# Kernel tuning notes

Measured on AMD Instinct MI355X. Metric: run time of the kernel, lower is better.

## Reference

```python
import jax, jax.numpy as jnp
import numpy as np

B, S, D, H, MLP_D = 2, 2048, 512, 8, 128
DH = D // H  # 64
EPS = 1e-5


def setup_inputs() -> dict:
    key = jax.random.key(0)
    ks = jax.random.split(key, 8)
    return {
        "z": jax.random.normal(ks[0], (B, S, D), dtype=jnp.float32),
        "head_w": jax.random.normal(ks[1], (H, D, 3 * DH), dtype=jnp.float32),
        "w_o": jax.random.normal(ks[2], (H * DH, D), dtype=jnp.float32),
        "ln_w": jnp.ones((D,), dtype=jnp.float32),
        "ln_b": jnp.zeros((D,), dtype=jnp.float32),
        "w1": jax.random.normal(ks[3], (D, MLP_D), dtype=jnp.float32) * (1.0 / np.sqrt(D)),
        "b1": jnp.zeros((MLP_D,), dtype=jnp.float32),
        "w2": jax.random.normal(ks[4], (MLP_D, D), dtype=jnp.float32) * (1.0 / np.sqrt(MLP_D)),
        "b2": jnp.zeros((D,), dtype=jnp.float32),
    }


def _layernorm(x, w, b):
    mu = jnp.mean(x, axis=-1, keepdims=True)
    var = jnp.var(x, axis=-1, keepdims=True)
    return (x - mu) * jax.lax.rsqrt(var + EPS) * w + b


def reference(z, head_w, w_o, ln_w, ln_b, w1, b1, w2, b2):
    # --- MSA block: z = MSA(LN(z)) + z ---
    x = _layernorm(z, ln_w, ln_b)                       # [B,S,D]
    qkv = jnp.einsum("bsd,hde->bhse", x, head_w)        # [B,H,S,3*DH]
    q, k, v = qkv[..., :DH], qkv[..., DH:2 * DH], qkv[..., 2 * DH:]
    scores = jnp.einsum("bhsd,bhtd->bhst", q, k) / jnp.sqrt(jnp.float32(DH))
    p = jax.nn.softmax(scores, axis=-1)                 # [B,H,S,S]
    o = jnp.einsum("bhst,bhtd->bhsd", p, v)             # [B,H,S,DH]
    # concat heads along last dim (head order matches torch.cat), then project
    o = jnp.transpose(o, (0, 2, 1, 3)).reshape(B, S, H * DH)
    z = o @ w_o + z
    # --- MLP block: z = GELU(Linear2(Linear1(LN(z)))) + z (GELU last, per Sequential) ---
    y = _layernorm(z, ln_w, ln_b)
    y = (y @ w1 + b1) @ w2 + b2
    z = jax.nn.gelu(y, approximate=False) + z
    return z
```

## Files before the change

### kernel.cpp

```cpp
#include <hip/hip_runtime.h>
#include <hip/hip_bf16.h>

typedef unsigned short u16;
typedef unsigned int u32;
typedef __attribute__((ext_vector_type(8))) short short8;
typedef __attribute__((ext_vector_type(8))) __bf16 bf16x8;
typedef __attribute__((ext_vector_type(4))) float f32x4;

#define DEV static __device__ __forceinline__

DEV float bf2f(u16 u) { unsigned v = ((unsigned)u) << 16; float f; __builtin_memcpy(&f, &v, 4); return f; }
DEV u16 f2bf(float f) {
  unsigned u; __builtin_memcpy(&u, &f, 4);
  unsigned lsb = (u >> 16) & 1;
  u += 0x7fffu + lsb;
  return (u16)(u >> 16);
}
DEV u16 tbf(float f) {
  unsigned u; __builtin_memcpy(&u, &f, 4);
  return (u16)(u >> 16);
}
DEV float exp2fast(float x) { return __builtin_amdgcn_exp2f(x); }
DEV f32x4 mfma16(short8 a, short8 b, f32x4 c) {
  return __builtin_amdgcn_mfma_f32_16x16x32_bf16(
      __builtin_bit_cast(bf16x8, a), __builtin_bit_cast(bf16x8, b), c, 0, 0, 0);
}
DEV short8 ld8(const u16* p) { return *(const short8*)p; }

__global__ void prep_all(const float* __restrict__ hw, const float* __restrict__ wo,
                         const float* __restrict__ w1, const float* __restrict__ w2,
                         u16* __restrict__ wqh, u16* __restrict__ wql,
                         u16* __restrict__ woT, u16* __restrict__ w1T, u16* __restrict__ w2T) {
  int idx = blockIdx.x * 256 + threadIdx.x;
  if (idx < 786432) {
    int e = idx % 192;
    int d = (idx / 192) % 512;
    int h = idx / (192 * 512);
    float v = hw[idx];
    int n = (e < 64) ? (h * 64 + e) : (e < 128) ? (512 + h * 64 + e - 64) : (1024 + h * 64 + e - 128);
    size_t oi = (size_t)n * 512 + d;
    u16 hh = f2bf(v);
    wqh[oi] = hh;
    if (e < 128) wql[oi] = f2bf(v - bf2f(hh));
  } else if (idx < 786432 + 262144) {
    int i = idx - 786432;
    int n = i % 512, k = i / 512;
    woT[(size_t)n * 512 + k] = f2bf(wo[i]);
  } else if (idx < 786432 + 262144 + 65536) {
    int i = idx - (786432 + 262144);
    int n = i % 128, k = i / 128;
    w1T[(size_t)n * 512 + k] = f2bf(w1[i]);
  } else if (idx < 786432 + 262144 + 131072) {
    int i = idx - (786432 + 262144 + 65536);
    int n = i % 512, k = i / 512;
    w2T[(size_t)n * 128 + k] = f2bf(w2[i]);
  }
}

__global__ __launch_bounds__(256) void ln_kernel(const float* __restrict__ in,
                                                 const float* __restrict__ w,
                                                 const float* __restrict__ bb,
                                                 u16* __restrict__ hi, u16* __restrict__ lo) {
  const int wv = threadIdx.x >> 6, lane = threadIdx.x & 63;
  const int row = blockIdx.x * 4 + wv;
  const float4* r = (const float4*)(in + (size_t)row * 512);
  float4 a0 = r[lane * 2], a1 = r[lane * 2 + 1];
  float s = a0.x + a0.y + a0.z + a0.w + a1.x + a1.y + a1.z + a1.w;
  float ss = a0.x * a0.x + a0.y * a0.y + a0.z * a0.z + a0.w * a0.w +
             a1.x * a1.x + a1.y * a1.y + a1.z * a1.z + a1.w * a1.w;
#pragma unroll
  for (int m = 1; m < 64; m <<= 1) { s += __shfl_xor(s, m); ss += __shfl_xor(ss, m); }
  float mu = s * (1.f / 512.f);
  float var = ss * (1.f / 512.f) - mu * mu;
  float rstd = rsqrtf(var + 1e-5f);
  const float4* wp = (const float4*)w + lane * 2;
  const float4* bp = (const float4*)bb + lane * 2;
  float4 w0 = wp[0], w1v = wp[1], b0 = bp[0], b1v = bp[1];
  float xv[8] = {a0.x, a0.y, a0.z, a0.w, a1.x, a1.y, a1.z, a1.w};
  float wv8[8] = {w0.x, w0.y, w0.z, w0.w, w1v.x, w1v.y, w1v.z, w1v.w};
  float bv8[8] = {b0.x, b0.y, b0.z, b0.w, b1v.x, b1v.y, b1v.z, b1v.w};
  short8 oh, ol;
#pragma unroll
  for (int i = 0; i < 8; i++) {
    float v = (xv[i] - mu) * rstd * wv8[i] + bv8[i];
    u16 hh = f2bf(v);
    oh[i] = (short)hh;
    ol[i] = (short)f2bf(v - bf2f(hh));
  }
  *(short8*)(hi + (size_t)row * 512 + lane * 8) = oh;
  *(short8*)(lo + (size_t)row * 512 + lane * 8) = ol;
}

__global__ __launch_bounds__(256) void gemm_qkv(const u16* __restrict__ Ah, const u16* __restrict__ Alo,
                                                const u16* __restrict__ Bh, const u16* __restrict__ Blo,
                                                u16* __restrict__ qkh, u16* __restrict__ qkl,
                                                u16* __restrict__ vT) {
  __shared__ __align__(16) u16 As[128][40], Asl[128][40], Bs[64][40], Bsl[64][40];
  const int tid = threadIdx.x, lane = tid & 63, wv = tid >> 6;
  const int wm = wv >> 1, wn = wv & 1, g = lane >> 4, r16 = lane & 15;
  const int bm = blockIdx.x * 128, bn = blockIdx.y * 64;
  const bool split = blockIdx.y < 16;
  short8 sA[2], sAl[2], sB, sBl;
  auto ldtile = [&](int kt) {
#pragma unroll
    for (int c = 0; c < 2; c++) {
      int ch = c * 256 + tid;
      sA[c] = ld8(Ah + (size_t)(bm + (ch >> 2)) * 512 + kt + (ch & 3) * 8);
      if (split) sAl[c] = ld8(Alo + (size_t)(bm + (ch >> 2)) * 512 + kt + (ch & 3) * 8);
    }
    sB = ld8(Bh + (size_t)(bn + (tid >> 2)) * 512 + kt + (tid & 3) * 8);
    if (split) sBl = ld8(Blo + (size_t)(bn + (tid >> 2)) * 512 + kt + (tid & 3) * 8);
  };
  f32x4 acc[4][2] = {};
  ldtile(0);
  for (int kt = 0; kt < 512; kt += 32) {
    __syncthreads();
#pragma unroll
    for (int c = 0; c < 2; c++) {
      int ch = c * 256 + tid;
      *(short8*)&As[ch >> 2][(ch & 3) * 8] = sA[c];
      if (split) *(short8*)&Asl[ch >> 2][(ch & 3) * 8] = sAl[c];
    }
    *(short8*)&Bs[tid >> 2][(tid & 3) * 8] = sB;
    if (split) *(short8*)&Bsl[tid >> 2][(tid & 3) * 8] = sBl;
    __syncthreads();
    if (kt + 32 < 512) ldtile(kt + 32);
    short8 af[4], bf_[2], afl[4], bfl[2];
#pragma unroll
    for (int mi = 0; mi < 4; mi++) af[mi] = *(const short8*)&As[wm * 64 + mi * 16 + r16][g * 8];
#pragma unroll
    for (int ni = 0; ni < 2; ni++) bf_[ni] = *(const short8*)&Bs[wn * 32 + ni * 16 + r16][g * 8];
    if (split) {
#pragma unroll
      for (int mi = 0; mi < 4; mi++) afl[mi] = *(const short8*)&Asl[wm * 64 + mi * 16 + r16][g * 8];
#pragma unroll
      for (int ni = 0; ni < 2; ni++) bfl[ni] = *(const short8*)&Bsl[wn * 32 + ni * 16 + r16][g * 8];
    }
#pragma unroll
    for (int mi = 0; mi < 4; mi++)
#pragma unroll
      for (int ni = 0; ni < 2; ni++) {
        acc[mi][ni] = mfma16(af[mi], bf_[ni], acc[mi][ni]);
        if (split) {
          acc[mi][ni] = mfma16(af[mi], bfl[ni], acc[mi][ni]);
          acc[mi][ni] = mfma16(afl[mi], bf_[ni], acc[mi][ni]);
        }
      }
  }
#pragma unroll
  for (int mi = 0; mi < 4; mi++)
#pragma unroll
    for (int ni = 0; ni < 2; ni++) {
      int col = bn + wn * 32 + ni * 16 + r16;
      int row0 = bm + wm * 64 + mi * 16 + g * 4;
      if (split) {
#pragma unroll
        for (int j = 0; j < 4; j++) {
          size_t oi = (size_t)(row0 + j) * 1024 + col;
          float v = acc[mi][ni][j];
          u16 hh = f2bf(v);
          qkh[oi] = hh;
          qkl[oi] = f2bf(v - bf2f(hh));
        }
      } else {
        int vcol = col - 1024;
        ushort4 pk;
        pk.x = f2bf(acc[mi][ni][0]);
        pk.y = f2bf(acc[mi][ni][1]);
        pk.z = f2bf(acc[mi][ni][2]);
        pk.w = f2bf(acc[mi][ni][3]);
        *(ushort4*)(vT + (size_t)vcol * 4096 + row0) = pk;
      }
    }
}

template <int MF, int NF, int EPI>
__global__ __launch_bounds__(256) void gemm_g(const u16* __restrict__ A, const u16* __restrict__ BT,
                                              const float* __restrict__ res, const float* __restrict__ bias,
                                              u16* __restrict__ outb, float* __restrict__ outf,
                                              int N, int K) {
  constexpr int BM = 32 * MF, BN = 32 * NF;
  constexpr int CA = (BM * 4 + 255) / 256, CB = (BN * 4 + 255) / 256;
  __shared__ __align__(16) u16 As[BM][40], Bs[BN][40];
  const int tid = threadIdx.x, lane = tid & 63, wv = tid >> 6;
  const int wm = wv >> 1, wn = wv & 1, g = lane >> 4, r16 = lane & 15;
  const int bm = blockIdx.x * BM, bn = blockIdx.y * BN;
  short8 sA[CA], sB[CB];
  auto ldtile = [&](int kt) {
#pragma unroll
    for (int c = 0; c < CA; c++) {
      int ch = c * 256 + tid;
      if (ch < BM * 4) sA[c] = ld8(A + (size_t)(bm + (ch >> 2)) * K + kt + (ch & 3) * 8);
    }
#pragma unroll
    for (int c = 0; c < CB; c++) {
      int ch = c * 256 + tid;
      if (ch < BN * 4) sB[c] = ld8(BT + (size_t)(bn + (ch >> 2)) * K + kt + (ch & 3) * 8);
    }
  };
  f32x4 acc[MF][NF] = {};
  ldtile(0);
  for (int kt = 0; kt < K; kt += 32) {
    __syncthreads();
#pragma unroll
    for (int c = 0; c < CA; c++) {
      int ch = c * 256 + tid;
      if (ch < BM * 4) *(short8*)&As[ch >> 2][(ch & 3) * 8] = sA[c];
    }
#pragma unroll
    for (int c = 0; c < CB; c++) {
      int ch = c * 256 + tid;
      if (ch < BN * 4) *(short8*)&Bs[ch >> 2][(ch & 3) * 8] = sB[c];
    }
    __syncthreads();
    if (kt + 32 < K) ldtile(kt + 32);
    short8 af[MF], bf_[NF];
#pragma unroll
    for (int mi = 0; mi < MF; mi++) af[mi] = *(const short8*)&As[wm * 16 * MF + mi * 16 + r16][g * 8];
#pragma unroll
    for (int ni = 0; ni < NF; ni++) bf_[ni] = *(const short8*)&Bs[wn * 16 * NF + ni * 16 + r16][g * 8];
#pragma unroll
    for (int mi = 0; mi < MF; mi++)
#pragma unroll
      for (int ni = 0; ni < NF; ni++) acc[mi][ni] = mfma16(af[mi], bf_[ni], acc[mi][ni]);
  }
#pragma unroll
  for (int mi = 0; mi < MF; mi++)
#pragma unroll
    for (int ni = 0; ni < NF; ni++) {
      int col = bn + wn * 16 * NF + ni * 16 + r16;
      int row0 = bm + wm * 16 * MF + mi * 16 + g * 4;
#pragma unroll
      for (int j = 0; j < 4; j++) {
        size_t oi = (size_t)(row0 + j) * N + col;
        float v = acc[mi][ni][j];
        if (EPI == 1) {
          outf[oi] = v + res[oi];
        } else if (EPI == 2) {
          outb[oi] = f2bf(v + bias[col]);
        } else {
          float u = v + bias[col];
          float gl = 0.5f * u * (1.0f + erff(u * 0.70710678118f));
          outf[oi] = gl + res[oi];
        }
      }
    }
}

__global__ __launch_bounds__(256) void attn_kernel(const u16* __restrict__ qkh,
                                                   const u16* __restrict__ qkl,
                                                   const u16* __restrict__ vT,
                                                   u16* __restrict__ o) {
  constexpr int SK = 72, SV = 136, SP = 136;
  __shared__ __align__(16) u16 Kh[128 * SK], Kl[128 * SK], Vt[64 * SV];
  __shared__ __align__(16) u16 Pl[4][16 * SP];
  const int tid = threadIdx.x, lane = tid & 63, w = tid >> 6;
  const int g = lane >> 4, r16 = lane & 15;
  const int qb = blockIdx.x * 64;
  const int b = blockIdx.y >> 3, h = blockIdx.y & 7;
  const size_t bbase = (size_t)b * 2048 * 1024;
  const u16* Qh = qkh + bbase + h * 64;
  const u16* Ql = qkl + bbase + h * 64;
  const u16* KgH = qkh + bbase + 512 + h * 64;
  const u16* KgL = qkl + bbase + 512 + h * 64;
  const u16* Vtg = vT + (size_t)h * 64 * 4096 + (size_t)b * 2048;

  const int qrow = qb + w * 16 + r16;
  short8 qh[2], qlo[2];
#pragma unroll
  for (int ks = 0; ks < 2; ks++) {
    qh[ks] = ld8(Qh + (size_t)qrow * 1024 + ks * 32 + g * 8);
    qlo[ks] = ld8(Ql + (size_t)qrow * 1024 + ks * 32 + g * 8);
  }

  f32x4 oacc[4] = {};
  float m_r = -3e38f, l_r = 0.f;

  const int vd0 = tid >> 4, vkv = (tid & 15) * 8;
  short8 kA[4], kB[4], vS[4];
  auto ldkv = [&](int kt) {
#pragma unroll
    for (int c = 0; c < 4; c++) {
      int ch = c * 256 + tid;
      int kr = ch >> 3, kc = (ch & 7) * 8;
      kA[c] = ld8(KgH + (size_t)(kt + kr) * 1024 + kc);
      kB[c] = ld8(KgL + (size_t)(kt + kr) * 1024 + kc);
    }
#pragma unroll
    for (int c = 0; c < 4; c++)
      vS[c] = ld8(Vtg + (size_t)(vd0 + c * 16) * 4096 + kt + vkv);
  };
  ldkv(0);

  for (int kt = 0; kt < 2048; kt += 128) {
    __syncthreads();
#pragma unroll
    for (int c = 0; c < 4; c++) {
      int ch = c * 256 + tid;
      int kr = ch >> 3, kc = (ch & 7) * 8;
      *(short8*)&Kh[kr * SK + kc] = kA[c];
      *(short8*)&Kl[kr * SK + kc] = kB[c];
    }
#pragma unroll
    for (int c = 0; c < 4; c++)
      *(short8*)&Vt[(vd0 + c * 16) * SV + vkv] = vS[c];
    __syncthreads();
    if (kt + 128 < 2048) ldkv(kt + 128);
    f32x4 s[8];
#pragma unroll
    for (int f = 0; f < 8; f++) {
      s[f] = f32x4{0.f, 0.f, 0.f, 0.f};
#pragma unroll
      for (int ks = 0; ks < 2; ks++) {
        short8 bh = *(const short8*)&Kh[(f * 16 + r16) * SK + ks * 32 + g * 8];
        short8 bl = *(const short8*)&Kl[(f * 16 + r16) * SK + ks * 32 + g * 8];
        s[f] = mfma16(bh, qh[ks], s[f]);
        s[f] = mfma16(bl, qh[ks], s[f]);
        s[f] = mfma16(bh, qlo[ks], s[f]);
      }
    }
    constexpr float SCL2 = 0.125f * 1.44269504f;
    float a[8][4];
    float vm = -3e38f;
#pragma unroll
    for (int f = 0; f < 8; f++)
#pragma unroll
      for (int r = 0; r < 4; r++) {
        a[f][r] = s[f][r] * SCL2;
        vm = fmaxf(vm, a[f][r]);
      }
    vm = fmaxf(vm, __shfl_xor(vm, 16));
    vm = fmaxf(vm, __shfl_xor(vm, 32));
    float mn = fmaxf(m_r, vm);
    float scl = exp2fast(m_r - mn);
    m_r = mn;
    float rs = 0.f;
#pragma unroll
    for (int f = 0; f < 8; f++) {
      float e0 = exp2fast(a[f][0] - mn), e1 = exp2fast(a[f][1] - mn);
      float e2 = exp2fast(a[f][2] - mn), e3 = exp2fast(a[f][3] - mn);
      rs += (e0 + e1) + (e2 + e3);
      u32 u0, u1, u2, u3;
      __builtin_memcpy(&u0, &e0, 4);
      __builtin_memcpy(&u1, &e1, 4);
      __builtin_memcpy(&u2, &e2, 4);
      __builtin_memcpy(&u3, &e3, 4);
      uint2 pk;
      pk.x = (u0 >> 16) | (u1 & 0xFFFF0000u);
      pk.y = (u2 >> 16) | (u3 & 0xFFFF0000u);
      *(uint2*)&Pl[w][r16 * SP + f * 16 + g * 4] = pk;
    }
    rs += __shfl_xor(rs, 16);
    rs += __shfl_xor(rs, 32);
    l_r = l_r * scl + rs;
#pragma unroll
    for (int j = 0; j < 4; j++) {
      float sj = __shfl(scl, (g << 4) + (g << 2) + j);
#pragma unroll
      for (int dt = 0; dt < 4; dt++) oacc[dt][j] *= sj;
    }
#pragma unroll
    for (int ks = 0; ks < 4; ks++) {
      short8 pa = *(const short8*)&Pl[w][r16 * SP + ks * 32 + g * 8];
#pragma unroll
      for (int dt = 0; dt < 4; dt++) {
        short8 vb = *(const short8*)&Vt[(dt * 16 + r16) * SV + ks * 32 + g * 8];
        oacc[dt] = mfma16(pa, vb, oacc[dt]);
      }
    }
  }
#pragma unroll
  for (int j = 0; j < 4; j++) {
    float lj = __shfl(l_r, (g << 4) + (g << 2) + j);
    float il = 1.f / lj;
    int row = b * 2048 + qb + w * 16 + g * 4 + j;
#pragma unroll
    for (int dt = 0; dt < 4; dt++) {
      int col = h * 64 + dt * 16 + r16;
      o[(size_t)row * 512 + col] = f2bf(oacc[dt][j] * il);
    }
  }
}

extern "C" void kernel_launch(void* const* d_in, const int* in_sizes, int n_in,
                              void* d_out, int out_size, void* d_ws, size_t ws_size,
                              hipStream_t stream) {
  const float* z = (const float*)d_in[0];
  const float* head_w = (const float*)d_in[1];
  const float* w_o = (const float*)d_in[2];
  const float* ln_w = (const float*)d_in[3];
  const float* ln_b = (const float*)d_in[4];
  const float* w1 = (const float*)d_in[5];
  const float* b1 = (const float*)d_in[6];
  const float* w2 = (const float*)d_in[7];
  const float* b2 = (const float*)d_in[8];
  float* out = (float*)d_out;

  size_t off = 0;
  auto alc = [&](size_t n) {
    void* p = (char*)d_ws + off;
    off += (n + 255) & ~(size_t)255;
    return p;
  };
  u16* x_hi = (u16*)alc((size_t)4096 * 512 * 2);
  u16* x_lo = (u16*)alc((size_t)4096 * 512 * 2);
  u16* wqh = (u16*)alc((size_t)1536 * 512 * 2);
  u16* wql = (u16*)alc((size_t)1536 * 512 * 2);
  u16* woT = (u16*)alc((size_t)512 * 512 * 2);
  u16* w1T = (u16*)alc((size_t)128 * 512 * 2);
  u16* w2T = (u16*)alc((size_t)512 * 128 * 2);
  u16* qkh = (u16*)alc((size_t)4096 * 1024 * 2);
  u16* qkl = (u16*)alc((size_t)4096 * 1024 * 2);
  u16* vT = (u16*)alc((size_t)512 * 4096 * 2);
  u16* ob = (u16*)alc((size_t)4096 * 512 * 2);
  float* z2 = (float*)alc((size_t)4096 * 512 * 4);
  u16* tb = (u16*)alc((size_t)4096 * 128 * 2);

  prep_all<<<4608, 256, 0, stream>>>(head_w, w_o, w1, w2, wqh, wql, woT, w1T, w2T);

  ln_kernel<<<1024, 256, 0, stream>>>(z, ln_w, ln_b, x_hi, x_lo);

  gemm_qkv<<<dim3(32, 24), 256, 0, stream>>>(x_hi, x_lo, wqh, wql, qkh, qkl, vT);

  attn_kernel<<<dim3(32, 16), 256, 0, stream>>>(qkh, qkl, vT, ob);

  gemm_g<2, 2, 1><<<dim3(64, 8), 256, 0, stream>>>(ob, woT, z, nullptr, nullptr, z2, 512, 512);

  ln_kernel<<<1024, 256, 0, stream>>>(z2, ln_w, ln_b, x_hi, x_lo);

  gemm_g<1, 2, 2><<<dim3(128, 2), 256, 0, stream>>>(x_hi, w1T, nullptr, b1, tb, nullptr, 128, 512);

  gemm_g<2, 2, 3><<<dim3(64, 8), 256, 0, stream>>>(tb, w2T, z2, b2, nullptr, out, 512, 128);
}
```

Measured before the change: 128.2 us.

## Process two query tiles per wave in attention to reuse K/V fragments

Attention blocks shrink from 4 waves to 2, and each wave now handles 32 query rows as two 16-row tiles. Each K and V fragment read from LDS then feeds two sets of MFMAs, halving LDS reads per MFMA. The cost is about double the accumulator and register pressure per wave, twice as many global loads per thread when staging K/V, and fewer waves per block to hide latency. Launch bounds are set to 128 threads with a minimum of 2 blocks.

```diff
diff --git a/kernel.cpp b/kernel.cpp
--- a/kernel.cpp
+++ b/kernel.cpp
@@ -14,10 +14,6 @@
   unsigned u; __builtin_memcpy(&u, &f, 4);
   unsigned lsb = (u >> 16) & 1;
   u += 0x7fffu + lsb;
-  return (u16)(u >> 16);
-}
-DEV u16 tbf(float f) {
-  unsigned u; __builtin_memcpy(&u, &f, 4);
   return (u16)(u >> 16);
 }
 DEV float exp2fast(float x) { return __builtin_amdgcn_exp2f(x); }
@@ -247,13 +243,13 @@
     }
 }
 
-__global__ __launch_bounds__(256) void attn_kernel(const u16* __restrict__ qkh,
-                                                   const u16* __restrict__ qkl,
-                                                   const u16* __restrict__ vT,
-                                                   u16* __restrict__ o) {
+__global__ __launch_bounds__(128, 2) void attn_kernel(const u16* __restrict__ qkh,
+                                                      const u16* __restrict__ qkl,
+                                                      const u16* __restrict__ vT,
+                                                      u16* __restrict__ o) {
   constexpr int SK = 72, SV = 136, SP = 136;
   __shared__ __align__(16) u16 Kh[128 * SK], Kl[128 * SK], Vt[64 * SV];
-  __shared__ __align__(16) u16 Pl[4][16 * SP];
+  __shared__ __align__(16) u16 Pl[2][32 * SP];
   const int tid = threadIdx.x, lane = tid & 63, w = tid >> 6;
   const int g = lane >> 4, r16 = lane & 15;
   const int qb = blockIdx.x * 64;
@@ -265,121 +261,142 @@
   const u16* KgL = qkl + bbase + 512 + h * 64;
   const u16* Vtg = vT + (size_t)h * 64 * 4096 + (size_t)b * 2048;
 
-  const int qrow = qb + w * 16 + r16;
-  short8 qh[2], qlo[2];
-#pragma unroll
-  for (int ks = 0; ks < 2; ks++) {
-    qh[ks] = ld8(Qh + (size_t)qrow * 1024 + ks * 32 + g * 8);
-    qlo[ks] = ld8(Ql + (size_t)qrow * 1024 + ks * 32 + g * 8);
-  }
-
-  f32x4 oacc[4] = {};
-  float m_r = -3e38f, l_r = 0.f;
-
-  const int vd0 = tid >> 4, vkv = (tid & 15) * 8;
-  short8 kA[4], kB[4], vS[4];
+  short8 qh[2][2], qlo[2][2];
+#pragma unroll
+  for (int t = 0; t < 2; t++) {
+    int qrow = qb + w * 32 + t * 16 + r16;
+#pragma unroll
+    for (int ks = 0; ks < 2; ks++) {
+      qh[t][ks] = ld8(Qh + (size_t)qrow * 1024 + ks * 32 + g * 8);
+      qlo[t][ks] = ld8(Ql + (size_t)qrow * 1024 + ks * 32 + g * 8);
+    }
+  }
+
+  f32x4 oacc[2][4] = {};
+  float m_r[2] = {-3e38f, -3e38f}, l_r[2] = {0.f, 0.f};
+
+  short8 kA[8], kB[8], vS[8];
   auto ldkv = [&](int kt) {
 #pragma unroll
-    for (int c = 0; c < 4; c++) {
-      int ch = c * 256 + tid;
-      int kr = ch >> 3, kc = (ch & 7) * 8;
+    for (int c = 0; c < 8; c++) {
+      int kr = c * 16 + (tid >> 3), kc = (tid & 7) * 8;
       kA[c] = ld8(KgH + (size_t)(kt + kr) * 1024 + kc);
       kB[c] = ld8(KgL + (size_t)(kt + kr) * 1024 + kc);
     }
 #pragma unroll
-    for (int c = 0; c < 4; c++)
-      vS[c] = ld8(Vtg + (size_t)(vd0 + c * 16) * 4096 + kt + vkv);
+    for (int c = 0; c < 8; c++) {
+      int vd = c * 8 + (tid >> 4), vc = (tid & 15) * 8;
+      vS[c] = ld8(Vtg + (size_t)vd * 4096 + kt + vc);
+    }
   };
   ldkv(0);
 
   for (int kt = 0; kt < 2048; kt += 128) {
     __syncthreads();
 #pragma unroll
-    for (int c = 0; c < 4; c++) {
-      int ch = c * 256 + tid;
-      int kr = ch >> 3, kc = (ch & 7) * 8;
+    for (int c = 0; c < 8; c++) {
+      int kr = c * 16 + (tid >> 3), kc = (tid & 7) * 8;
       *(short8*)&Kh[kr * SK + kc] = kA[c];
       *(short8*)&Kl[kr * SK + kc] = kB[c];
     }
 #pragma unroll
-    for (int c = 0; c < 4; c++)
-      *(short8*)&Vt[(vd0 + c * 16) * SV + vkv] = vS[c];
+    for (int c = 0; c < 8; c++) {
+      int vd = c * 8 + (tid >> 4), vc = (tid & 15) * 8;
+      *(short8*)&Vt[vd * SV + vc] = vS[c];
+    }
     __syncthreads();
     if (kt + 128 < 2048) ldkv(kt + 128);
-    f32x4 s[8];
+    f32x4 s[2][8];
+#pragma unroll
+    for (int t = 0; t < 2; t++)
+#pragma unroll
+      for (int f = 0; f < 8; f++) s[t][f] = f32x4{0.f, 0.f, 0.f, 0.f};
 #pragma unroll
     for (int f = 0; f < 8; f++) {
-      s[f] = f32x4{0.f, 0.f, 0.f, 0.f};
+      int krow = f * 16 + r16;
 #pragma unroll
       for (int ks = 0; ks < 2; ks++) {
-        short8 bh = *(const short8*)&Kh[(f * 16 + r16) * SK + ks * 32 + g * 8];
-        short8 bl = *(const short8*)&Kl[(f * 16 + r16) * SK + ks * 32 + g * 8];
-        s[f] = mfma16(bh, qh[ks], s[f]);
-        s[f] = mfma16(bl, qh[ks], s[f]);
-        s[f] = mfma16(bh, qlo[ks], s[f]);
+        short8 bh = *(const short8*)&Kh[krow * SK + ks * 32 + g * 8];
+        short8 bl = *(const short8*)&Kl[krow * SK + ks * 32 + g * 8];
+#pragma unroll
+        for (int t = 0; t < 2; t++) {
+          s[t][f] = mfma16(bh, qh[t][ks], s[t][f]);
+          s[t][f] = mfma16(bl, qh[t][ks], s[t][f]);
+          s[t][f] = mfma16(bh, qlo[t][ks], s[t][f]);
+        }
       }
     }
     constexpr float SCL2 = 0.125f * 1.44269504f;
-    float a[8][4];
-    float vm = -3e38f;
-#pragma unroll
-    for (int f = 0; f < 8; f++)
-#pragma unroll
-      for (int r = 0; r < 4; r++) {
-        a[f][r] = s[f][r] * SCL2;
-        vm = fmaxf(vm, a[f][r]);
-      }
-    vm = fmaxf(vm, __shfl_xor(vm, 16));
-    vm = fmaxf(vm, __shfl_xor(vm, 32));
-    float mn = fmaxf(m_r, vm);
-    float scl = exp2fast(m_r - mn);
-    m_r = mn;
-    float rs = 0.f;
-#pragma unroll
-    for (int f = 0; f < 8; f++) {
-      float e0 = exp2fast(a[f][0] - mn), e1 = exp2fast(a[f][1] - mn);
-      float e2 = exp2fast(a[f][2] - mn), e3 = exp2fast(a[f][3] - mn);
-      rs += (e0 + e1) + (e2 + e3);
-      u32 u0, u1, u2, u3;
-      __builtin_memcpy(&u0, &e0, 4);
-      __builtin_memcpy(&u1, &e1, 4);
-      __builtin_memcpy(&u2, &e2, 4);
-      __builtin_memcpy(&u3, &e3, 4);
-      uint2 pk;
-      pk.x = (u0 >> 16) | (u1 & 0xFFFF0000u);
-      pk.y = (u2 >> 16) | (u3 & 0xFFFF0000u);
-      *(uint2*)&Pl[w][r16 * SP + f * 16 + g * 4] = pk;
-    }
-    rs += __shfl_xor(rs, 16);
-    rs += __shfl_xor(rs, 32);
-    l_r = l_r * scl + rs;
-#pragma unroll
-    for (int j = 0; j < 4; j++) {
-      float sj = __shfl(scl, (g << 4) + (g << 2) + j);
-#pragma unroll
-      for (int dt = 0; dt < 4; dt++) oacc[dt][j] *= sj;
-    }
+    float scl[2];
+#pragma unroll
+    for (int t = 0; t < 2; t++) {
+      float a[8][4];
+      float vm = -3e38f;
+#pragma unroll
+      for (int f = 0; f < 8; f++)
+#pragma unroll
+        for (int r = 0; r < 4; r++) {
+          a[f][r] = s[t][f][r] * SCL2;
+          vm = fmaxf(vm, a[f][r]);
+        }
+      vm = fmaxf(vm, __shfl_xor(vm, 16));
+      vm = fmaxf(vm, __shfl_xor(vm, 32));
+      float mn = fmaxf(m_r[t], vm);
+      scl[t] = exp2fast(m_r[t] - mn);
+      m_r[t] = mn;
+      float rs = 0.f;
+#pragma unroll
+      for (int f = 0; f < 8; f++) {
+        float e0 = exp2fast(a[f][0] - mn), e1 = exp2fast(a[f][1] - mn);
+        float e2 = exp2fast(a[f][2] - mn), e3 = exp2fast(a[f][3] - mn);
+        rs += (e0 + e1) + (e2 + e3);
+        u32 u0, u1, u2, u3;
+        __builtin_memcpy(&u0, &e0, 4);
+        __builtin_memcpy(&u1, &e1, 4);
+        __builtin_memcpy(&u2, &e2, 4);
+        __builtin_memcpy(&u3, &e3, 4);
+        uint2 pk;
+        pk.x = (u0 >> 16) | (u1 & 0xFFFF0000u);
+        pk.y = (u2 >> 16) | (u3 & 0xFFFF0000u);
+        *(uint2*)&Pl[w][(t * 16 + r16) * SP + f * 16 + g * 4] = pk;
+      }
+      rs += __shfl_xor(rs, 16);
+      rs += __shfl_xor(rs, 32);
+      l_r[t] = l_r[t] * scl[t] + rs;
+    }
+#pragma unroll
+    for (int t = 0; t < 2; t++)
+#pragma unroll
+      for (int j = 0; j < 4; j++) {
+        float sj = __shfl(scl[t], (g << 4) + (g << 2) + j);
+#pragma unroll
+        for (int dt = 0; dt < 4; dt++) oacc[t][dt][j] *= sj;
+      }
 #pragma unroll
     for (int ks = 0; ks < 4; ks++) {
-      short8 pa = *(const short8*)&Pl[w][r16 * SP + ks * 32 + g * 8];
+      short8 pa0 = *(const short8*)&Pl[w][(0 * 16 + r16) * SP + ks * 32 + g * 8];
+      short8 pa1 = *(const short8*)&Pl[w][(1 * 16 + r16) * SP + ks * 32 + g * 8];
 #pragma unroll
       for (int dt = 0; dt < 4; dt++) {
         short8 vb = *(const short8*)&Vt[(dt * 16 + r16) * SV + ks * 32 + g * 8];
-        oacc[dt] = mfma16(pa, vb, oacc[dt]);
-      }
-    }
-  }
-#pragma unroll
-  for (int j = 0; j < 4; j++) {
-    float lj = __shfl(l_r, (g << 4) + (g << 2) + j);
-    float il = 1.f / lj;
-    int row = b * 2048 + qb + w * 16 + g * 4 + j;
-#pragma unroll
-    for (int dt = 0; dt < 4; dt++) {
-      int col = h * 64 + dt * 16 + r16;
-      o[(size_t)row * 512 + col] = f2bf(oacc[dt][j] * il);
-    }
-  }
+        oacc[0][dt] = mfma16(pa0, vb, oacc[0][dt]);
+        oacc[1][dt] = mfma16(pa1, vb, oacc[1][dt]);
+      }
+    }
+  }
+#pragma unroll
+  for (int t = 0; t < 2; t++)
+#pragma unroll
+    for (int j = 0; j < 4; j++) {
+      float lj = __shfl(l_r[t], (g << 4) + (g << 2) + j);
+      float il = 1.f / lj;
+      int row = b * 2048 + qb + w * 32 + t * 16 + g * 4 + j;
+#pragma unroll
+      for (int dt = 0; dt < 4; dt++) {
+        int col = h * 64 + dt * 16 + r16;
+        o[(size_t)row * 512 + col] = f2bf(oacc[t][dt][j] * il);
+      }
+    }
 }
 
 extern "C" void kernel_launch(void* const* d_in, const int* in_sizes, int n_in,
@@ -422,7 +439,7 @@
 
   gemm_qkv<<<dim3(32, 24), 256, 0, stream>>>(x_hi, x_lo, wqh, wql, qkh, qkl, vT);
 
-  attn_kernel<<<dim3(32, 16), 256, 0, stream>>>(qkh, qkl, vT, ob);
+  attn_kernel<<<dim3(32, 16), 128, 0, stream>>>(qkh, qkl, vT, ob);
 
   gemm_g<2, 2, 1><<<dim3(64, 8), 256, 0, stream>>>(ob, woT, z, nullptr, nullptr, z2, 512, 512);
 
```

New measurement: 139.3 us. +8.6%, slower.
